# Performance work log

Hardware: AMD Instinct MI355X
Metric: run time of the kernel (lower is better)

## Reference

```python
import jax, jax.numpy as jnp
import numpy as np

HIDDEN = 1024
INTER = 4096
EPS = 1e-12


def _ste(q, x):
    # straight-through estimator: forward q, backward identity wrt x
    return x + jax.lax.stop_gradient(q - x)


def setup_inputs() -> dict:
    key = jax.random.key(0)
    ks = jax.random.split(key, 4)
    hidden_states = jax.random.normal(ks[0], (4, 2048, INTER), dtype=jnp.float32)
    input_tensor = jax.random.normal(ks[1], (4, 2048, HIDDEN), dtype=jnp.float32)
    W = jax.random.normal(ks[2], (HIDDEN, INTER), dtype=jnp.float32) * 0.02
    b = jnp.zeros((HIDDEN,), dtype=jnp.float32)
    clip_val = jnp.asarray(2.5, dtype=jnp.float32)  # learnable elastic alpha
    gamma = jnp.ones((HIDDEN,), dtype=jnp.float32)
    beta = jnp.zeros((HIDDEN,), dtype=jnp.float32)
    return {"hidden_states": hidden_states, "input_tensor": input_tensor,
            "W": W, "b": b, "clip_val": clip_val, "gamma": gamma, "beta": beta}


def reference(hidden_states, input_tensor, W, b, clip_val, gamma, beta):
    # --- binary weight (BWN): per-output-channel scale = mean(|W|, axis=in) ---
    w_scale = jnp.mean(jnp.abs(W), axis=1, keepdims=True)  # [hidden, 1]
    W_q = _ste(w_scale * jnp.sign(W), W)                    # [hidden, inter]
    # --- elastic signed binary activation: q = alpha * sign(x / alpha) ---
    s = hidden_states / clip_val
    x_q = clip_val * _ste(jnp.sign(s), s)                   # [b, s, inter]
    # --- dense projection ---
    h = jnp.einsum('bsi,hi->bsh', x_q, W_q) + b             # [b, s, hidden]
    # dropout prob 0.0 (eval mode) -> no-op
    # --- residual + LayerNorm (eps=1e-12) ---
    r = h + input_tensor
    mu = jnp.mean(r, axis=-1, keepdims=True)
    var = jnp.mean(jnp.square(r - mu), axis=-1, keepdims=True)
    out = (r - mu) * jax.lax.rsqrt(var + EPS) * gamma + beta
    return out
```

## Files before the change

### kernel.cpp

```cpp
#include <hip/hip_runtime.h>
#include <stdint.h>

#define HIDDEN 1024
#define INTER  4096
#define NWORDS 64
#define NCHUNK 16
#define ROWS   8192
#define MT     8
#define GBLK   (ROWS / MT)

typedef unsigned long long u64;


__global__ __launch_bounds__(256)
void pack_w_kernel(const float* __restrict__ W, u64* __restrict__ wbits_t,
                   float* __restrict__ wscale) {
    int h    = blockIdx.x;
    int lane = threadIdx.x & 63;
    int wave = threadIdx.x >> 6;
    const float4* row = (const float4*)(W + (size_t)h * INTER);
    float asum = 0.f;
    #pragma unroll
    for (int c = wave; c < NCHUNK; c += 4) {
        float4 v = row[c * 64 + lane];
        asum += fabsf(v.x) + fabsf(v.y) + fabsf(v.z) + fabsf(v.w);
        u64 b0 = __ballot(v.x < 0.0f);
        u64 b1 = __ballot(v.y < 0.0f);
        u64 b2 = __ballot(v.z < 0.0f);
        u64 b3 = __ballot(v.w < 0.0f);
        if (lane == 0) {
            u64* dst = wbits_t + (size_t)(4 * c) * HIDDEN + h;
            dst[0 * HIDDEN] = b0;
            dst[1 * HIDDEN] = b1;
            dst[2 * HIDDEN] = b2;
            dst[3 * HIDDEN] = b3;
        }
    }
    #pragma unroll
    for (int off = 32; off > 0; off >>= 1) asum += __shfl_down(asum, off);
    __shared__ float red[4];
    if (lane == 0) red[wave] = asum;
    __syncthreads();
    if (threadIdx.x == 0)
        wscale[h] = (red[0] + red[1] + red[2] + red[3]) * (1.0f / INTER);
}

__global__ __launch_bounds__(256, 4)
void main_kernel(const float* __restrict__ hs, const u64* __restrict__ wbits_t,
                 const float* __restrict__ wscale, const float* __restrict__ bias,
                 const float* __restrict__ clipp, const float* __restrict__ input,
                 const float* __restrict__ gamma, const float* __restrict__ beta,
                 float* __restrict__ out) {
    int t    = threadIdx.x;
    int lane = t & 63;
    int wave = t >> 6;
    int m0   = blockIdx.x * MT;

    __shared__ u64 sA[MT][NWORDS];

    #pragma unroll
    for (int r = 0; r < 2; ++r) {
        int mi = wave * 2 + r;
        const float4* row = (const float4*)(hs + (size_t)(m0 + mi) * INTER);
        #pragma unroll
        for (int c = 0; c < NCHUNK; ++c) {
            float4 v = row[c * 64 + lane];
            u64 b0 = __ballot(v.x < 0.0f);
            u64 b1 = __ballot(v.y < 0.0f);
            u64 b2 = __ballot(v.z < 0.0f);
            u64 b3 = __ballot(v.w < 0.0f);
            if (lane == 0) {
                sA[mi][4 * c + 0] = b0;
                sA[mi][4 * c + 1] = b1;
                sA[mi][4 * c + 2] = b2;
                sA[mi][4 * c + 3] = b3;
            }
        }
    }
    __syncthreads();

    int h0 = t * 4;
    int acc[MT][4];
    #pragma unroll
    for (int mi = 0; mi < MT; ++mi)
        #pragma unroll
        for (int c = 0; c < 4; ++c) acc[mi][c] = 0;

    #pragma unroll 2
    for (int k = 0; k < NWORDS; ++k) {
        const u64* wp = wbits_t + (size_t)k * HIDDEN + h0;
        ulonglong2 wA = ((const ulonglong2*)wp)[0];
        ulonglong2 wB = ((const ulonglong2*)wp)[1];
        #pragma unroll
        for (int mi = 0; mi < MT; ++mi) {
            u64 a  = sA[mi][k];
            u64 x0 = a ^ wA.x;
            u64 x1 = a ^ wA.y;
            u64 x2 = a ^ wB.x;
            u64 x3 = a ^ wB.y;
            acc[mi][0] += __popc((uint32_t)x0) + __popc((uint32_t)(x0 >> 32));
            acc[mi][1] += __popc((uint32_t)x1) + __popc((uint32_t)(x1 >> 32));
            acc[mi][2] += __popc((uint32_t)x2) + __popc((uint32_t)(x2 >> 32));
            acc[mi][3] += __popc((uint32_t)x3) + __popc((uint32_t)(x3 >> 32));
        }
    }

    float clip = clipp[0];
    float4 cw = reinterpret_cast<const float4*>(wscale)[t];
    cw.x *= clip; cw.y *= clip; cw.z *= clip; cw.w *= clip;
    float4 bi = reinterpret_cast<const float4*>(bias)[t];
    float4 gm = reinterpret_cast<const float4*>(gamma)[t];
    float4 bt = reinterpret_cast<const float4*>(beta)[t];

    float vals[MT][4];
    #pragma unroll
    for (int mi = 0; mi < MT; ++mi) {
        float4 inp = reinterpret_cast<const float4*>(input + (size_t)(m0 + mi) * HIDDEN)[t];
        vals[mi][0] = fmaf((float)(INTER - 2 * acc[mi][0]), cw.x, bi.x + inp.x);
        vals[mi][1] = fmaf((float)(INTER - 2 * acc[mi][1]), cw.y, bi.y + inp.y);
        vals[mi][2] = fmaf((float)(INTER - 2 * acc[mi][2]), cw.z, bi.z + inp.z);
        vals[mi][3] = fmaf((float)(INTER - 2 * acc[mi][3]), cw.w, bi.w + inp.w);
    }

    __shared__ float red_s[4][MT];
    __shared__ float red_q[4][MT];
    __shared__ float s_mu[MT], s_rs[MT];
    #pragma unroll
    for (int mi = 0; mi < MT; ++mi) {
        float s = vals[mi][0] + vals[mi][1] + vals[mi][2] + vals[mi][3];
        float q = vals[mi][0] * vals[mi][0] + vals[mi][1] * vals[mi][1]
                + vals[mi][2] * vals[mi][2] + vals[mi][3] * vals[mi][3];
        #pragma unroll
        for (int off = 32; off > 0; off >>= 1) {
            s += __shfl_down(s, off);
            q += __shfl_down(q, off);
        }
        if (lane == 0) { red_s[wave][mi] = s; red_q[wave][mi] = q; }
    }
    __syncthreads();
    if (t < MT) {
        float s = red_s[0][t] + red_s[1][t] + red_s[2][t] + red_s[3][t];
        float q = red_q[0][t] + red_q[1][t] + red_q[2][t] + red_q[3][t];
        float mu  = s * (1.0f / HIDDEN);
        float var = fmaf(-mu, mu, q * (1.0f / HIDDEN));
        s_mu[t] = mu;
        s_rs[t] = rsqrtf(var + 1e-12f);
    }
    __syncthreads();

    #pragma unroll
    for (int mi = 0; mi < MT; ++mi) {
        float mu = s_mu[mi], rs = s_rs[mi];
        float4 o;
        o.x = (vals[mi][0] - mu) * rs * gm.x + bt.x;
        o.y = (vals[mi][1] - mu) * rs * gm.y + bt.y;
        o.z = (vals[mi][2] - mu) * rs * gm.z + bt.z;
        o.w = (vals[mi][3] - mu) * rs * gm.w + bt.w;
        reinterpret_cast<float4*>(out + (size_t)(m0 + mi) * HIDDEN)[t] = o;
    }
}

extern "C" void kernel_launch(void* const* d_in, const int* in_sizes, int n_in,
                              void* d_out, int out_size, void* d_ws, size_t ws_size,
                              hipStream_t stream) {
    const float* hs    = (const float*)d_in[0];
    const float* inp   = (const float*)d_in[1];
    const float* W     = (const float*)d_in[2];
    const float* b     = (const float*)d_in[3];
    const float* clip  = (const float*)d_in[4];
    const float* gamma = (const float*)d_in[5];
    const float* beta  = (const float*)d_in[6];
    float* out = (float*)d_out;

    u64*   wbits  = (u64*)d_ws;
    float* wscale = (float*)((char*)d_ws + (size_t)NWORDS * HIDDEN * 8);

    pack_w_kernel<<<HIDDEN, 256, 0, stream>>>(W, wbits, wscale);
    main_kernel<<<GBLK, 256, 0, stream>>>(hs, wbits, wscale, b, clip,
                                          inp, gamma, beta, out);
}
```

Measured before the change: 315.0 us.

## Replace XOR-popcount binary GEMM with int8 MFMA on ±1 signs

```diff
diff --git a/kernel.cpp b/kernel.cpp
--- a/kernel.cpp
+++ b/kernel.cpp
@@ -3,160 +3,201 @@
 
 #define HIDDEN 1024
 #define INTER  4096
-#define NWORDS 64
-#define NCHUNK 16
 #define ROWS   8192
-#define MT     8
-#define GBLK   (ROWS / MT)
-
-typedef unsigned long long u64;
-
+#define BM     32
+#define BK     64
+#define NKSTEP (INTER / BK)
+#define NBLK   (ROWS / BM)
+#define BTILE  (HIDDEN * BK)
+
+typedef int i32x4 __attribute__((ext_vector_type(4)));
+typedef const uint32_t __attribute__((address_space(1))) gu32;
+typedef uint32_t __attribute__((address_space(3))) lu32;
+
+__device__ __forceinline__ uint32_t sgn4(float4 v) {
+    uint32_t b0 = (v.x < 0.f) ? 0xFFu : 0x01u;
+    uint32_t b1 = (v.y < 0.f) ? 0xFFu : 0x01u;
+    uint32_t b2 = (v.z < 0.f) ? 0xFFu : 0x01u;
+    uint32_t b3 = (v.w < 0.f) ? 0xFFu : 0x01u;
+    return b0 | (b1 << 8) | (b2 << 16) | (b3 << 24);
+}
 
 __global__ __launch_bounds__(256)
-void pack_w_kernel(const float* __restrict__ W, u64* __restrict__ wbits_t,
+void pack_w_kernel(const float* __restrict__ W, uint8_t* __restrict__ Bg,
                    float* __restrict__ wscale) {
-    int h    = blockIdx.x;
-    int lane = threadIdx.x & 63;
-    int wave = threadIdx.x >> 6;
+    int h = blockIdx.x;
+    int tid = threadIdx.x;
+    int lane = tid & 63, wv = tid >> 6;
     const float4* row = (const float4*)(W + (size_t)h * INTER);
     float asum = 0.f;
     #pragma unroll
-    for (int c = wave; c < NCHUNK; c += 4) {
-        float4 v = row[c * 64 + lane];
+    for (int q = 0; q < 4; ++q) {
+        int g = q * 256 + tid;
+        float4 v = row[g];
         asum += fabsf(v.x) + fabsf(v.y) + fabsf(v.z) + fabsf(v.w);
-        u64 b0 = __ballot(v.x < 0.0f);
-        u64 b1 = __ballot(v.y < 0.0f);
-        u64 b2 = __ballot(v.z < 0.0f);
-        u64 b3 = __ballot(v.w < 0.0f);
-        if (lane == 0) {
-            u64* dst = wbits_t + (size_t)(4 * c) * HIDDEN + h;
-            dst[0 * HIDDEN] = b0;
-            dst[1 * HIDDEN] = b1;
-            dst[2 * HIDDEN] = b2;
-            dst[3 * HIDDEN] = b3;
-        }
+        int tt = g >> 4;
+        *(uint32_t*)(Bg + (size_t)tt * BTILE + h * BK + (g & 15) * 4) = sgn4(v);
     }
     #pragma unroll
     for (int off = 32; off > 0; off >>= 1) asum += __shfl_down(asum, off);
     __shared__ float red[4];
-    if (lane == 0) red[wave] = asum;
-    __syncthreads();
-    if (threadIdx.x == 0)
-        wscale[h] = (red[0] + red[1] + red[2] + red[3]) * (1.0f / INTER);
-}
-
-__global__ __launch_bounds__(256, 4)
-void main_kernel(const float* __restrict__ hs, const u64* __restrict__ wbits_t,
+    if (lane == 0) red[wv] = asum;
+    __syncthreads();
+    if (tid == 0) wscale[h] = (red[0] + red[1] + red[2] + red[3]) * (1.0f / INTER);
+}
+
+__global__ __launch_bounds__(512, 2)
+void main_kernel(const float* __restrict__ hs, const uint8_t* __restrict__ Bg,
                  const float* __restrict__ wscale, const float* __restrict__ bias,
                  const float* __restrict__ clipp, const float* __restrict__ input,
                  const float* __restrict__ gamma, const float* __restrict__ beta,
                  float* __restrict__ out) {
-    int t    = threadIdx.x;
-    int lane = t & 63;
-    int wave = t >> 6;
-    int m0   = blockIdx.x * MT;
-
-    __shared__ u64 sA[MT][NWORDS];
-
-    #pragma unroll
-    for (int r = 0; r < 2; ++r) {
-        int mi = wave * 2 + r;
-        const float4* row = (const float4*)(hs + (size_t)(m0 + mi) * INTER);
-        #pragma unroll
-        for (int c = 0; c < NCHUNK; ++c) {
-            float4 v = row[c * 64 + lane];
-            u64 b0 = __ballot(v.x < 0.0f);
-            u64 b1 = __ballot(v.y < 0.0f);
-            u64 b2 = __ballot(v.z < 0.0f);
-            u64 b3 = __ballot(v.w < 0.0f);
-            if (lane == 0) {
-                sA[mi][4 * c + 0] = b0;
-                sA[mi][4 * c + 1] = b1;
-                sA[mi][4 * c + 2] = b2;
-                sA[mi][4 * c + 3] = b3;
+    __shared__ alignas(16) uint8_t sB[2 * BTILE];
+    __shared__ alignas(16) uint8_t sA[2][BM * BK];
+    __shared__ float red_s[8][BM], red_q[8][BM];
+    __shared__ float s_mu[BM], s_rs[BM];
+
+    const int tid  = threadIdx.x;
+    const int lane = tid & 63;
+    const int wave = tid >> 6;
+    const int m0   = blockIdx.x * BM;
+
+    const int ar = tid >> 4;
+    const int ac = tid & 15;
+    const int aofs = ar * BK + ac * 4;
+    const float* aload_base = hs + (size_t)(m0 + ar) * INTER + ac * 4;
+
+    const int l15 = lane & 15;
+    const int kc  = lane >> 4;
+    int aro[2], bro[8];
+    #pragma unroll
+    for (int rt = 0; rt < 2; ++rt) aro[rt] = (rt * 16 + l15) * BK + kc * 16;
+    #pragma unroll
+    for (int ct = 0; ct < 8; ++ct)
+        bro[ct] = (wave * 128 + ct * 16 + l15) * BK + kc * 16;
+
+    i32x4 acc[2][8];
+    #pragma unroll
+    for (int rt = 0; rt < 2; ++rt)
+        #pragma unroll
+        for (int ct = 0; ct < 8; ++ct) acc[rt][ct] = (i32x4){0, 0, 0, 0};
+
+    {
+        float4 av = *(const float4*)(aload_base);
+        const uint8_t* gs = Bg + wave * 8192 + lane * 16;
+        uint8_t* ld = &sB[wave * 8192];
+        #pragma unroll
+        for (int j = 0; j < 8; ++j)
+            __builtin_amdgcn_global_load_lds((gu32*)(gs + j * 1024),
+                                             (lu32*)(ld + j * 1024), 16, 0, 0);
+        *(uint32_t*)&sA[0][aofs] = sgn4(av);
+    }
+    __syncthreads();
+
+    for (int t = 0; t < NKSTEP; ++t) {
+        const int cur = t & 1;
+        const int nxt = cur ^ 1;
+        const bool more = (t + 1 < NKSTEP);
+        float4 av;
+        if (more) {
+            av = *(const float4*)(aload_base + (t + 1) * BK);
+            const uint8_t* gs = Bg + (size_t)(t + 1) * BTILE + wave * 8192 + lane * 16;
+            uint8_t* ld = &sB[nxt * BTILE + wave * 8192];
+            #pragma unroll
+            for (int j = 0; j < 8; ++j)
+                __builtin_amdgcn_global_load_lds((gu32*)(gs + j * 1024),
+                                                 (lu32*)(ld + j * 1024), 16, 0, 0);
+        }
+        const uint8_t* bb = &sB[cur * BTILE];
+        i32x4 a0 = *(const i32x4*)&sA[cur][aro[0]];
+        i32x4 a1 = *(const i32x4*)&sA[cur][aro[1]];
+        #pragma unroll
+        for (int ct = 0; ct < 8; ++ct) {
+            i32x4 bf = *(const i32x4*)&bb[bro[ct]];
+            acc[0][ct] = __builtin_amdgcn_mfma_i32_16x16x64_i8(a0, bf, acc[0][ct], 0, 0, 0);
+            acc[1][ct] = __builtin_amdgcn_mfma_i32_16x16x64_i8(a1, bf, acc[1][ct], 0, 0, 0);
+        }
+        if (more) *(uint32_t*)&sA[nxt][aofs] = sgn4(av);
+        __syncthreads();
+    }
+
+    float clip = clipp[0];
+    float cw[8], bi[8];
+    const int hb = wave * 128 + l15;
+    #pragma unroll
+    for (int ct = 0; ct < 8; ++ct) {
+        cw[ct] = clip * wscale[hb + ct * 16];
+        bi[ct] = bias[hb + ct * 16];
+    }
+    float* yl = (float*)sB;
+    float sp[2][4] = {}, qp[2][4] = {};
+    const int rb = (lane >> 4) * 4;
+    #pragma unroll
+    for (int rt = 0; rt < 2; ++rt) {
+        #pragma unroll
+        for (int ct = 0; ct < 8; ++ct) {
+            int hcol = hb + ct * 16;
+            #pragma unroll
+            for (int rg = 0; rg < 4; ++rg) {
+                int rl = rt * 16 + rb + rg;
+                float v = fmaf((float)acc[rt][ct][rg], cw[ct],
+                               bi[ct] + input[(size_t)(m0 + rl) * HIDDEN + hcol]);
+                sp[rt][rg] += v;
+                qp[rt][rg] += v * v;
+                yl[rl * HIDDEN + hcol] = v;
             }
         }
     }
-    __syncthreads();
-
-    int h0 = t * 4;
-    int acc[MT][4];
-    #pragma unroll
-    for (int mi = 0; mi < MT; ++mi)
-        #pragma unroll
-        for (int c = 0; c < 4; ++c) acc[mi][c] = 0;
-
-    #pragma unroll 2
-    for (int k = 0; k < NWORDS; ++k) {
-        const u64* wp = wbits_t + (size_t)k * HIDDEN + h0;
-        ulonglong2 wA = ((const ulonglong2*)wp)[0];
-        ulonglong2 wB = ((const ulonglong2*)wp)[1];
-        #pragma unroll
-        for (int mi = 0; mi < MT; ++mi) {
-            u64 a  = sA[mi][k];
-            u64 x0 = a ^ wA.x;
-            u64 x1 = a ^ wA.y;
-            u64 x2 = a ^ wB.x;
-            u64 x3 = a ^ wB.y;
-            acc[mi][0] += __popc((uint32_t)x0) + __popc((uint32_t)(x0 >> 32));
-            acc[mi][1] += __popc((uint32_t)x1) + __popc((uint32_t)(x1 >> 32));
-            acc[mi][2] += __popc((uint32_t)x2) + __popc((uint32_t)(x2 >> 32));
-            acc[mi][3] += __popc((uint32_t)x3) + __popc((uint32_t)(x3 >> 32));
-        }
-    }
-
-    float clip = clipp[0];
-    float4 cw = reinterpret_cast<const float4*>(wscale)[t];
-    cw.x *= clip; cw.y *= clip; cw.z *= clip; cw.w *= clip;
-    float4 bi = reinterpret_cast<const float4*>(bias)[t];
-    float4 gm = reinterpret_cast<const float4*>(gamma)[t];
-    float4 bt = reinterpret_cast<const float4*>(beta)[t];
-
-    float vals[MT][4];
-    #pragma unroll
-    for (int mi = 0; mi < MT; ++mi) {
-        float4 inp = reinterpret_cast<const float4*>(input + (size_t)(m0 + mi) * HIDDEN)[t];
-        vals[mi][0] = fmaf((float)(INTER - 2 * acc[mi][0]), cw.x, bi.x + inp.x);
-        vals[mi][1] = fmaf((float)(INTER - 2 * acc[mi][1]), cw.y, bi.y + inp.y);
-        vals[mi][2] = fmaf((float)(INTER - 2 * acc[mi][2]), cw.z, bi.z + inp.z);
-        vals[mi][3] = fmaf((float)(INTER - 2 * acc[mi][3]), cw.w, bi.w + inp.w);
-    }
-
-    __shared__ float red_s[4][MT];
-    __shared__ float red_q[4][MT];
-    __shared__ float s_mu[MT], s_rs[MT];
-    #pragma unroll
-    for (int mi = 0; mi < MT; ++mi) {
-        float s = vals[mi][0] + vals[mi][1] + vals[mi][2] + vals[mi][3];
-        float q = vals[mi][0] * vals[mi][0] + vals[mi][1] * vals[mi][1]
-                + vals[mi][2] * vals[mi][2] + vals[mi][3] * vals[mi][3];
-        #pragma unroll
-        for (int off = 32; off > 0; off >>= 1) {
-            s += __shfl_down(s, off);
-            q += __shfl_down(q, off);
-        }
-        if (lane == 0) { red_s[wave][mi] = s; red_q[wave][mi] = q; }
-    }
-    __syncthreads();
-    if (t < MT) {
-        float s = red_s[0][t] + red_s[1][t] + red_s[2][t] + red_s[3][t];
-        float q = red_q[0][t] + red_q[1][t] + red_q[2][t] + red_q[3][t];
-        float mu  = s * (1.0f / HIDDEN);
-        float var = fmaf(-mu, mu, q * (1.0f / HIDDEN));
-        s_mu[t] = mu;
-        s_rs[t] = rsqrtf(var + 1e-12f);
-    }
-    __syncthreads();
-
-    #pragma unroll
-    for (int mi = 0; mi < MT; ++mi) {
-        float mu = s_mu[mi], rs = s_rs[mi];
+    #pragma unroll
+    for (int off = 1; off <= 8; off <<= 1) {
+        #pragma unroll
+        for (int rt = 0; rt < 2; ++rt)
+            #pragma unroll
+            for (int rg = 0; rg < 4; ++rg) {
+                sp[rt][rg] += __shfl_xor(sp[rt][rg], off);
+                qp[rt][rg] += __shfl_xor(qp[rt][rg], off);
+            }
+    }
+    if (l15 == 0) {
+        int g = lane >> 4;
+        #pragma unroll
+        for (int rt = 0; rt < 2; ++rt)
+            #pragma unroll
+            for (int rg = 0; rg < 4; ++rg) {
+                red_s[wave][rt * 16 + g * 4 + rg] = sp[rt][rg];
+                red_q[wave][rt * 16 + g * 4 + rg] = qp[rt][rg];
+            }
+    }
+    __syncthreads();
+    if (tid < BM) {
+        float ss = 0.f, qq = 0.f;
+        #pragma unroll
+        for (int w = 0; w < 8; ++w) { ss += red_s[w][tid]; qq += red_q[w][tid]; }
+        float mu  = ss * (1.0f / HIDDEN);
+        float var = fmaf(-mu, mu, qq * (1.0f / HIDDEN));
+        s_mu[tid] = mu;
+        s_rs[tid] = rsqrtf(var + 1e-12f);
+    }
+    __syncthreads();
+
+    const float4* gmp = (const float4*)gamma;
+    const float4* btp = (const float4*)beta;
+    const float4* yv  = (const float4*)yl;
+    float4* outp = (float4*)(out + (size_t)m0 * HIDDEN);
+    #pragma unroll
+    for (int j = 0; j < 16; ++j) {
+        int f  = j * 512 + tid;
+        int rl = f >> 8;
+        int c4 = f & 255;
+        float4 y4 = yv[f];
+        float4 g4 = gmp[c4], b4 = btp[c4];
+        float mu = s_mu[rl], rs = s_rs[rl];
         float4 o;
-        o.x = (vals[mi][0] - mu) * rs * gm.x + bt.x;
-        o.y = (vals[mi][1] - mu) * rs * gm.y + bt.y;
-        o.z = (vals[mi][2] - mu) * rs * gm.z + bt.z;
-        o.w = (vals[mi][3] - mu) * rs * gm.w + bt.w;
-        reinterpret_cast<float4*>(out + (size_t)(m0 + mi) * HIDDEN)[t] = o;
+        o.x = (y4.x - mu) * rs * g4.x + b4.x;
+        o.y = (y4.y - mu) * rs * g4.y + b4.y;
+        o.z = (y4.z - mu) * rs * g4.z + b4.z;
+        o.w = (y4.w - mu) * rs * g4.w + b4.w;
+        outp[f] = o;
     }
 }
 
@@ -172,10 +213,10 @@
     const float* beta  = (const float*)d_in[6];
     float* out = (float*)d_out;
 
-    u64*   wbits  = (u64*)d_ws;
-    float* wscale = (float*)((char*)d_ws + (size_t)NWORDS * HIDDEN * 8);
-
-    pack_w_kernel<<<HIDDEN, 256, 0, stream>>>(W, wbits, wscale);
-    main_kernel<<<GBLK, 256, 0, stream>>>(hs, wbits, wscale, b, clip,
+    uint8_t* Bg   = (uint8_t*)d_ws;
+    float* wscale = (float*)((char*)d_ws + (size_t)NKSTEP * BTILE);
+
+    pack_w_kernel<<<HIDDEN, 256, 0, stream>>>(W, Bg, wscale);
+    main_kernel<<<NBLK, 512, 0, stream>>>(hs, Bg, wscale, b, clip,
                                           inp, gamma, beta, out);
 }
```

Measured after the change: 320.5 us. Within noise of the previous version (+1.7%).
